# Optimization experiments

Hardware: AMD Instinct MI355X
Metric: run time of the kernel (lower is better)

The kernel has to match this reference:

```python
import jax, jax.numpy as jnp
import numpy as np

EPS = 1e-5

def layer_norm(x, alpha, beta):
    mean = jnp.mean(x, axis=-1, keepdims=True)
    var = jnp.mean(jnp.square(x - mean), axis=-1, keepdims=True)
    return alpha * ((x - mean) / jnp.sqrt(var + EPS)) + beta

def setup_inputs() -> dict:
    key = jax.random.key(0)
    B, S, D, H = 4, 2048, 1024, 16
    Dff = 4 * D
    ks = jax.random.split(key, 8)
    inp = {
        "x": jax.random.normal(ks[0], (B, S, D), jnp.float32),
        "attention_mask": jnp.ones((B, S), jnp.int32),
        "ln1_alpha": jnp.ones((D,), jnp.float32),
        "ln1_beta": jnp.zeros((D,), jnp.float32),
        "ln2_alpha": jnp.ones((D,), jnp.float32),
        "ln2_beta": jnp.zeros((D,), jnp.float32),
        "Wq": jax.random.normal(ks[1], (D, D), jnp.float32) * 0.05,
        "Wk": jax.random.normal(ks[2], (D, D), jnp.float32) * 0.05,
        "Wv": jax.random.normal(ks[3], (D, D), jnp.float32) * 0.05,
        "Wo": jax.random.normal(ks[4], (D, D), jnp.float32) * 0.05,
        "W1": jax.random.normal(ks[5], (D, Dff), jnp.float32) * 0.02,
        "b1": jnp.zeros((Dff,), jnp.float32),
        "W2": jax.random.normal(ks[6], (Dff, D), jnp.float32) * 0.02,
        "b2": jnp.zeros((D,), jnp.float32),
    }
    return inp

def reference(x, attention_mask, ln1_alpha, ln1_beta, ln2_alpha, ln2_beta,
              Wq, Wk, Wv, Wo, W1, b1, W2, b2):
    B, S, D = x.shape
    H = 16
    dh = D // H

    # LN1 + self-attention
    y = layer_norm(x, ln1_alpha, ln1_beta)
    Q = (y @ Wq).reshape(B, S, H, dh).transpose(0, 2, 1, 3)  # [B,H,S,dh]
    K = (y @ Wk).reshape(B, S, H, dh).transpose(0, 2, 1, 3)
    V = (y @ Wv).reshape(B, S, H, dh).transpose(0, 2, 1, 3)

    scores = jnp.einsum("bhqd,bhkd->bhqk", Q, K) / jnp.sqrt(jnp.float32(dh))
    causal = jnp.tril(jnp.ones((S, S), jnp.float32))  # [S,S]
    tmask = attention_mask.astype(jnp.float32)  # [B,S]
    amask = causal[None, None, :, :] * tmask[:, None, None, :] * tmask[:, None, :, None]
    scores = jnp.where(amask > 0, scores, jnp.float32(-1e30))
    attn = jax.nn.softmax(scores, axis=-1)
    # dropout omitted (deterministic inference)
    ctx = jnp.einsum("bhqk,bhkd->bhqd", attn, V)
    ctx = ctx.transpose(0, 2, 1, 3).reshape(B, S, D)
    x = x + ctx @ Wo

    # LN2 + GELU FFN
    y = layer_norm(x, ln2_alpha, ln2_beta)
    h = jax.nn.gelu(y @ W1 + b1, approximate=False)
    x = x + (h @ W2 + b2)
    return x
```

## Files before the change

kernel.cpp:

```cpp
#include <hip/hip_runtime.h>
#include <math.h>

typedef unsigned short u16;
typedef unsigned int u32;
typedef __attribute__((ext_vector_type(4))) unsigned short u16x4;
typedef __attribute__((ext_vector_type(8))) short bf16x8;
typedef __attribute__((ext_vector_type(4))) float f32x4;

#define B_ 4
#define S_ 2048
#define D_ 1024
#define H_ 16
#define NT (B_*S_)
#define DFF 4096

static __device__ __forceinline__ float bf2f(u16 u) {
    return __uint_as_float(((u32)u) << 16);
}
static __device__ __forceinline__ u16 f2bf(float f) {
    u32 u = __float_as_uint(f);
    u32 r = (u + 0x7fffu + ((u >> 16) & 1u)) >> 16;
    return (u16)r;
}
static __device__ __forceinline__ void gload_lds16(const void* g, void* l) {
    __builtin_amdgcn_global_load_lds(
        (const __attribute__((address_space(1))) void*)g,
        (__attribute__((address_space(3))) void*)l, 16, 0, 0);
}
static __device__ __forceinline__ float gelu_fast(float x) {
    float x2 = x * x;
    float u = x * fmaf(0.044715f, x2, 1.0f);
    float e = exp2f(2.3022079f * u);
    float r = __builtin_amdgcn_rcpf(e + 1.0f);
    return x - x * r;
}

#define MBAR() do { asm volatile("" ::: "memory"); \
                    __builtin_amdgcn_s_barrier(); \
                    asm volatile("" ::: "memory"); } while (0)

__global__ void transpose_f2b4(const float* __restrict__ s0, const float* __restrict__ s1,
                               const float* __restrict__ s2, const float* __restrict__ s3,
                               u16* __restrict__ d0, u16* __restrict__ d1,
                               u16* __restrict__ d2, u16* __restrict__ d3,
                               int R, int C) {
    const float* in = s0; u16* out = d0;
    if (blockIdx.z == 1) { in = s1; out = d1; }
    else if (blockIdx.z == 2) { in = s2; out = d2; }
    else if (blockIdx.z == 3) { in = s3; out = d3; }
    __shared__ float t[32][33];
    int c0 = blockIdx.x * 32, r0 = blockIdx.y * 32;
    int x = threadIdx.x, y = threadIdx.y;
    #pragma unroll
    for (int i = 0; i < 4; i++)
        t[y + i*8][x] = in[(long)(r0 + y + i*8) * C + c0 + x];
    __syncthreads();
    #pragma unroll
    for (int i = 0; i < 4; i++)
        out[(long)(c0 + y + i*8) * R + r0 + x] = f2bf(t[x][y + i*8]);
}

__global__ void transpose_f2b(const float* __restrict__ in, u16* __restrict__ out,
                              int R, int C) {
    __shared__ float t[32][33];
    int c0 = blockIdx.x * 32, r0 = blockIdx.y * 32;
    int x = threadIdx.x, y = threadIdx.y;
    #pragma unroll
    for (int i = 0; i < 4; i++)
        t[y + i*8][x] = in[(long)(r0 + y + i*8) * C + c0 + x];
    __syncthreads();
    #pragma unroll
    for (int i = 0; i < 4; i++)
        out[(long)(c0 + y + i*8) * R + r0 + x] = f2bf(t[x][y + i*8]);
}

__global__ void transpose_v(const u16* __restrict__ V, u16* __restrict__ Vt) {
    __shared__ u16 t[32][33];
    int z = blockIdx.z; int b = z >> 4, h = z & 15;
    int s0 = blockIdx.x * 32, d0 = blockIdx.y * 32;
    int x = threadIdx.x, y = threadIdx.y;
    const u16* in = V + ((long)b * S_ + s0) * D_ + h * 64 + d0;
    #pragma unroll
    for (int i = 0; i < 4; i++)
        t[y + i*8][x] = in[(long)(y + i*8) * D_ + x];
    __syncthreads();
    u16* out = Vt + ((long)z * 64 + d0) * S_ + s0;
    #pragma unroll
    for (int i = 0; i < 4; i++)
        out[(long)(y + i*8) * S_ + x] = t[x][y + i*8];
}

__global__ __launch_bounds__(256) void ln_kernel(
    const float* __restrict__ X, const float* __restrict__ alpha,
    const float* __restrict__ beta, u16* __restrict__ Y) {
    int row = blockIdx.x, tid = threadIdx.x;
    float4 xv = ((const float4*)(X + (long)row * D_))[tid];
    float v[4] = {xv.x, xv.y, xv.z, xv.w};
    float s = 0.f, ss = 0.f;
    #pragma unroll
    for (int i = 0; i < 4; i++) { s += v[i]; ss += v[i]*v[i]; }
    #pragma unroll
    for (int off = 32; off >= 1; off >>= 1) {
        s += __shfl_xor(s, off);
        ss += __shfl_xor(ss, off);
    }
    __shared__ float red[8];
    __shared__ float stats[2];
    int w = tid >> 6;
    if ((tid & 63) == 0) { red[w] = s; red[4 + w] = ss; }
    __syncthreads();
    if (tid == 0) {
        float S = red[0] + red[1] + red[2] + red[3];
        float SS = red[4] + red[5] + red[6] + red[7];
        float mean = S * (1.f / D_);
        float var = SS * (1.f / D_) - mean * mean;
        stats[0] = mean; stats[1] = rsqrtf(var + 1e-5f);
    }
    __syncthreads();
    float mean = stats[0], rstd = stats[1];
    float4 av = ((const float4*)alpha)[tid];
    float4 bv = ((const float4*)beta)[tid];
    u16x4 o;
    o[0] = f2bf((v[0] - mean) * rstd * av.x + bv.x);
    o[1] = f2bf((v[1] - mean) * rstd * av.y + bv.y);
    o[2] = f2bf((v[2] - mean) * rstd * av.z + bv.z);
    o[3] = f2bf((v[3] - mean) * rstd * av.w + bv.w);
    *(u16x4*)(Y + (long)row * D_ + tid * 4) = o;
}

#define BM 128
#define BN 128
#define BK 64

__global__ __launch_bounds__(256, 3) void gemm_bt(
    const u16* __restrict__ A,
    const u16* __restrict__ Bt0, const u16* __restrict__ Bt1, const u16* __restrict__ Bt2,
    void* __restrict__ C0, void* __restrict__ C1, void* __restrict__ C2,
    int M, int N, int K, int mode,
    const float* __restrict__ bias, const float* __restrict__ resid) {
    const u16* Bt = Bt0; void* C = C0;
    if (blockIdx.z == 1) { Bt = Bt1; C = C1; }
    else if (blockIdx.z == 2) { Bt = Bt2; C = C2; }

    __shared__ __align__(16) u16 Asm[BM * BK];
    __shared__ __align__(16) u16 Bsm[BN * BK];

    int tid = threadIdx.x;
    int lane = tid & 63, wave = tid >> 6;
    int l15 = lane & 15, quad = lane >> 4;
    int wm = wave & 1, wn = wave >> 1;
    long tm0 = (long)blockIdx.y * BM, tn0 = (long)blockIdx.x * BN;

    int srow = lane >> 3;
    int scol = (lane & 7) * 8;

    f32x4 acc[4][4] = {};

    for (int k0 = 0; k0 < K; k0 += BK) {
        __syncthreads();
        #pragma unroll
        for (int c = 0; c < 4; c++) {
            int chunk = wave * 4 + c;
            int row = chunk * 8 + srow;
            gload_lds16(&A[(tm0 + row) * (long)K + k0 + scol], &Asm[chunk * 512]);
            gload_lds16(&Bt[(tn0 + row) * (long)K + k0 + scol], &Bsm[chunk * 512]);
        }
        __syncthreads();
        #pragma unroll
        for (int ks = 0; ks < 2; ks++) {
            bf16x8 af[4], bfm[4];
            #pragma unroll
            for (int mt = 0; mt < 4; mt++)
                af[mt] = *(const bf16x8*)&Asm[(wm*64 + mt*16 + l15) * BK + ks*32 + quad*8];
            #pragma unroll
            for (int nt = 0; nt < 4; nt++)
                bfm[nt] = *(const bf16x8*)&Bsm[(wn*64 + nt*16 + l15) * BK + ks*32 + quad*8];
            #pragma unroll
            for (int mt = 0; mt < 4; mt++)
                #pragma unroll
                for (int nt = 0; nt < 4; nt++)
                    acc[mt][nt] = __builtin_amdgcn_mfma_f32_16x16x32_bf16(
                        af[mt], bfm[nt], acc[mt][nt], 0, 0, 0);
        }
    }

    #pragma unroll
    for (int mt = 0; mt < 4; mt++) {
        #pragma unroll
        for (int nt = 0; nt < 4; nt++) {
            #pragma unroll
            for (int i = 0; i < 4; i++) {
                long r = tm0 + wm*64 + mt*16 + quad*4 + i;
                long cn = tn0 + wn*64 + nt*16 + l15;
                long idx = r * N + cn;
                float val = acc[mt][nt][i];
                if (mode == 0) {
                    ((u16*)C)[idx] = f2bf(val);
                } else if (mode == 1) {
                    ((float*)C)[idx] = val + resid[idx];
                } else if (mode == 2) {
                    val += bias[cn];
                    ((u16*)C)[idx] = f2bf(gelu_fast(val));
                } else {
                    ((float*)C)[idx] = val + bias[cn] + resid[idx];
                }
            }
        }
    }
}

#define BM2 256
#define BN2 256
#define BK2 64

__global__ __launch_bounds__(512, 2) void gemm8p(
    const u16* __restrict__ A, const u16* __restrict__ Bt,
    u16* __restrict__ C0, u16* __restrict__ C1, u16* __restrict__ C2,
    int N, int K, int mode, const float* __restrict__ bias) {
    __shared__ __align__(16) u16 lds[2 * 32768];

    int tid = threadIdx.x;
    int lane = tid & 63, wave = tid >> 6;
    int l15 = lane & 15, quad = lane >> 4;
    int wm = wave & 1, wn = wave >> 1;
    long tm0 = (long)blockIdx.y * BM2, tn0 = (long)blockIdx.x * BN2;
    int srow = lane >> 3;
    int scolw = ((lane & 7) ^ srow) * 8;
    int sk = l15 & 7;
    int ca0 = ((quad) ^ sk) * 8;
    int ca1 = ((4 + quad) ^ sk) * 8;
    int steps = K >> 6;

    auto STAGE = [&](int kt, int half, int buf) {
        long kk = (long)kt * BK2;
        #pragma unroll
        for (int c = 0; c < 2; c++) {
            int chunk = wave * 2 + c;
            int rloc = (half & 1) * 128 + chunk * 8 + srow;
            const u16* g = (half < 2)
                ? &A [(tm0 + rloc) * (long)K + kk + scolw]
                : &Bt[(tn0 + rloc) * (long)K + kk + scolw];
            u16* l = &lds[buf * 32768 + (half >= 2 ? 16384 : 0)
                          + (half & 1) * 8192 + chunk * 512];
            gload_lds16(g, l);
        }
    };

    f32x4 acc[8][4] = {};
    bf16x8 af[4][2], bl[2][2], bh[2][2];

    STAGE(0, 0, 0); STAGE(0, 1, 0); STAGE(0, 2, 0); STAGE(0, 3, 0);
    if (steps > 1) { STAGE(1, 2, 1); STAGE(1, 3, 1); }
    if (steps > 1) asm volatile("s_waitcnt vmcnt(4)" ::: "memory");
    else           asm volatile("s_waitcnt vmcnt(0)" ::: "memory");
    MBAR();

    for (int t = 0; t < steps; ++t) {
        int cur = t & 1;
        const u16* Ab = &lds[cur * 32768];
        const u16* Bb = &lds[cur * 32768 + 16384];
        bool pf1 = (t + 1 < steps), pf2 = (t + 2 < steps);

        #pragma unroll
        for (int mt = 0; mt < 4; mt++) {
            int row = wm*128 + mt*16 + l15;
            af[mt][0] = *(const bf16x8*)&Ab[row * BK2 + ca0];
            af[mt][1] = *(const bf16x8*)&Ab[row * BK2 + ca1];
        }
        #pragma unroll
        for (int nt = 0; nt < 2; nt++) {
            int row = wn*64 + nt*16 + l15;
            bl[nt][0] = *(const bf16x8*)&Bb[row * BK2 + ca0];
            bl[nt][1] = *(const bf16x8*)&Bb[row * BK2 + ca1];
        }
        if (pf1) STAGE(t + 1, 0, cur ^ 1);
        MBAR();
        __builtin_amdgcn_s_setprio(1);
        #pragma unroll
        for (int mt = 0; mt < 4; mt++)
            #pragma unroll
            for (int nt = 0; nt < 2; nt++) {
                acc[mt][nt] = __builtin_amdgcn_mfma_f32_16x16x32_bf16(af[mt][0], bl[nt][0], acc[mt][nt], 0,0,0);
                acc[mt][nt] = __builtin_amdgcn_mfma_f32_16x16x32_bf16(af[mt][1], bl[nt][1], acc[mt][nt], 0,0,0);
            }
        __builtin_amdgcn_s_setprio(0);
        MBAR();

        #pragma unroll
        for (int nt = 0; nt < 2; nt++) {
            int row = wn*64 + (2+nt)*16 + l15;
            bh[nt][0] = *(const bf16x8*)&Bb[row * BK2 + ca0];
            bh[nt][1] = *(const bf16x8*)&Bb[row * BK2 + ca1];
        }
        if (pf1) STAGE(t + 1, 1, cur ^ 1);
        MBAR();
        __builtin_amdgcn_s_setprio(1);
        #pragma unroll
        for (int mt = 0; mt < 4; mt++)
            #pragma unroll
            for (int nt = 0; nt < 2; nt++) {
                acc[mt][2+nt] = __builtin_amdgcn_mfma_f32_16x16x32_bf16(af[mt][0], bh[nt][0], acc[mt][2+nt], 0,0,0);
                acc[mt][2+nt] = __builtin_amdgcn_mfma_f32_16x16x32_bf16(af[mt][1], bh[nt][1], acc[mt][2+nt], 0,0,0);
            }
        __builtin_amdgcn_s_setprio(0);
        MBAR();

        #pragma unroll
        for (int mt = 0; mt < 4; mt++) {
            int row = wm*128 + 64 + mt*16 + l15;
            af[mt][0] = *(const bf16x8*)&Ab[row * BK2 + ca0];
            af[mt][1] = *(const bf16x8*)&Ab[row * BK2 + ca1];
        }
        if (pf2) STAGE(t + 2, 2, cur);
        MBAR();
        __builtin_amdgcn_s_setprio(1);
        #pragma unroll
        for (int mt = 0; mt < 4; mt++)
            #pragma unroll
            for (int nt = 0; nt < 2; nt++) {
                acc[4+mt][2+nt] = __builtin_amdgcn_mfma_f32_16x16x32_bf16(af[mt][0], bh[nt][0], acc[4+mt][2+nt], 0,0,0);
                acc[4+mt][2+nt] = __builtin_amdgcn_mfma_f32_16x16x32_bf16(af[mt][1], bh[nt][1], acc[4+mt][2+nt], 0,0,0);
            }
        __builtin_amdgcn_s_setprio(0);
        MBAR();

        if (pf2) STAGE(t + 2, 3, cur);
        MBAR();
        __builtin_amdgcn_s_setprio(1);
        #pragma unroll
        for (int mt = 0; mt < 4; mt++)
            #pragma unroll
            for (int nt = 0; nt < 2; nt++) {
                acc[4+mt][nt] = __builtin_amdgcn_mfma_f32_16x16x32_bf16(af[mt][0], bl[nt][0], acc[4+mt][nt], 0,0,0);
                acc[4+mt][nt] = __builtin_amdgcn_mfma_f32_16x16x32_bf16(af[mt][1], bl[nt][1], acc[4+mt][nt], 0,0,0);
            }
        __builtin_amdgcn_s_setprio(0);
        if (pf2) asm volatile("s_waitcnt vmcnt(4)" ::: "memory");
        else     asm volatile("s_waitcnt vmcnt(0)" ::: "memory");
        MBAR();
    }

    #pragma unroll
    for (int mt = 0; mt < 8; mt++) {
        #pragma unroll
        for (int nt = 0; nt < 4; nt++) {
            #pragma unroll
            for (int i = 0; i < 4; i++) {
                long r = tm0 + wm*128 + mt*16 + quad*4 + i;
                int cn = (int)tn0 + wn*64 + nt*16 + l15;
                float val = acc[mt][nt][i];
                if (mode == 0) {
                    int mi = cn >> 10;
                    int col = cn & 1023;
                    u16* base = (mi == 0) ? C0 : (mi == 1 ? C1 : C2);
                    base[r * 1024 + col] = f2bf(val);
                } else {
                    val += bias[cn];
                    C0[r * (long)N + cn] = f2bf(gelu_fast(val));
                }
            }
        }
    }
}

#define LDP 72

__global__ __launch_bounds__(128, 2) void attn_kernel(
    const u16* __restrict__ Q, const u16* __restrict__ Kg, const u16* __restrict__ Vt,
    const int* __restrict__ mask, u16* __restrict__ O) {
    __shared__ __align__(16) u16 Psm[2][32 * LDP];
    int tid = threadIdx.x;
    int lane = tid & 63, wave = tid >> 6;
    int l15 = lane & 15, quad = lane >> 4;
    int bh = blockIdx.x; int b = bh >> 4, h = bh & 15;
    int j = blockIdx.y * 2 + wave;
    long tokBase = (long)b * S_;
    const float SCL = 0.125f * 1.4426950408889634f;
    const float MMAX = 20.0f;

    const bf16x8 ones = {16256,16256,16256,16256,16256,16256,16256,16256};
    u16* Pw = Psm[wave];
    const int* mb = mask + b * S_;

    #pragma unroll
    for (int half = 0; half < 2; half++) {
        int t = half ? (63 - j) : j;
        int q0 = t * 32;

        bf16x8 aq[2][2];
        #pragma unroll
        for (int mt = 0; mt < 2; mt++) {
            const u16* qptr = Q + (tokBase + q0 + mt*16 + l15) * D_ + h * 64;
            aq[mt][0] = *(const bf16x8*)(qptr + quad * 8);
            aq[mt][1] = *(const bf16x8*)(qptr + 32 + quad * 8);
        }

        f32x4 o[2][4] = {};
        f32x4 lacc[2] = {};
        int ktiles = t / 2 + 1;

        bf16x8 kb[4][2];
        #pragma unroll
        for (int nt = 0; nt < 4; nt++) {
            const u16* kp = Kg + (tokBase + nt*16 + l15) * D_ + h * 64;
            kb[nt][0] = *(const bf16x8*)(kp + quad * 8);
            kb[nt][1] = *(const bf16x8*)(kp + 32 + quad * 8);
        }

        for (int kt = 0; kt < ktiles; kt++) {
            int k0 = kt * 64;
            bf16x8 vb[4][2];
            #pragma unroll
            for (int d = 0; d < 4; d++) {
                const u16* vp = Vt + ((long)bh * 64 + d*16 + l15) * S_ + k0;
                vb[d][0] = *(const bf16x8*)(vp + quad * 8);
                vb[d][1] = *(const bf16x8*)(vp + 32 + quad * 8);
            }

            f32x4 s[2][4] = {};
            #pragma unroll
            for (int nt = 0; nt < 4; nt++) {
                s[0][nt] = __builtin_amdgcn_mfma_f32_16x16x32_bf16(aq[0][0], kb[nt][0], s[0][nt], 0,0,0);
                s[0][nt] = __builtin_amdgcn_mfma_f32_16x16x32_bf16(aq[0][1], kb[nt][1], s[0][nt], 0,0,0);
                s[1][nt] = __builtin_amdgcn_mfma_f32_16x16x32_bf16(aq[1][0], kb[nt][0], s[1][nt], 0,0,0);
                s[1][nt] = __builtin_amdgcn_mfma_f32_16x16x32_bf16(aq[1][1], kb[nt][1], s[1][nt], 0,0,0);
            }

            int k1 = (kt + 1 < ktiles) ? k0 + 64 : k0;
            bf16x8 kbn[4][2];
            #pragma unroll
            for (int nt = 0; nt < 4; nt++) {
                const u16* kp = Kg + (tokBase + k1 + nt*16 + l15) * D_ + h * 64;
                kbn[nt][0] = *(const bf16x8*)(kp + quad * 8);
                kbn[nt][1] = *(const bf16x8*)(kp + 32 + quad * 8);
            }

            int mk = 0;
            #pragma unroll
            for (int nt = 0; nt < 4; nt++)
                if (mb[k0 + nt*16 + l15] != 0) mk |= (1 << nt);

            #pragma unroll
            for (int mt = 0; mt < 2; mt++) {
                #pragma unroll
                for (int i = 0; i < 4; i++) {
                    int qq = q0 + mt*16 + quad*4 + i;
                    #pragma unroll
                    for (int nt = 0; nt < 4; nt++) {
                        int kc = k0 + nt*16 + l15;
                        float p = exp2f(fmaf(s[mt][nt][i], SCL, -MMAX));
                        p = (kc <= qq && ((mk >> nt) & 1)) ? p : 0.f;
                        Pw[(mt*16 + quad*4 + i) * LDP + nt*16 + l15] = f2bf(p);
                    }
                }
            }
            asm volatile("s_waitcnt lgkmcnt(0)" ::: "memory");

            #pragma unroll
            for (int hv = 0; hv < 2; hv++) {
                bf16x8 ap0 = *(const bf16x8*)&Pw[l15 * LDP + hv*32 + quad*8];
                bf16x8 ap1 = *(const bf16x8*)&Pw[(16 + l15) * LDP + hv*32 + quad*8];
                #pragma unroll
                for (int d = 0; d < 4; d++) {
                    o[0][d] = __builtin_amdgcn_mfma_f32_16x16x32_bf16(ap0, vb[d][hv], o[0][d], 0,0,0);
                    o[1][d] = __builtin_amdgcn_mfma_f32_16x16x32_bf16(ap1, vb[d][hv], o[1][d], 0,0,0);
                }
                lacc[0] = __builtin_amdgcn_mfma_f32_16x16x32_bf16(ap0, ones, lacc[0], 0,0,0);
                lacc[1] = __builtin_amdgcn_mfma_f32_16x16x32_bf16(ap1, ones, lacc[1], 0,0,0);
            }

            #pragma unroll
            for (int nt = 0; nt < 4; nt++) {
                kb[nt][0] = kbn[nt][0];
                kb[nt][1] = kbn[nt][1];
            }
        }

        #pragma unroll
        for (int mt = 0; mt < 2; mt++) {
            #pragma unroll
            for (int i = 0; i < 4; i++) {
                float inv = 1.f / lacc[mt][i];
                long r = tokBase + q0 + mt*16 + quad*4 + i;
                #pragma unroll
                for (int d = 0; d < 4; d++)
                    O[r * D_ + h*64 + d*16 + l15] = f2bf(o[mt][d][i] * inv);
            }
        }
    }
}

extern "C" void kernel_launch(void* const* d_in, const int* in_sizes, int n_in,
                              void* d_out, int out_size, void* d_ws, size_t ws_size,
                              hipStream_t stream) {
    const float* x    = (const float*)d_in[0];
    const int*   am   = (const int*)d_in[1];
    const float* ln1a = (const float*)d_in[2];
    const float* ln1b = (const float*)d_in[3];
    const float* ln2a = (const float*)d_in[4];
    const float* ln2b = (const float*)d_in[5];
    const float* wq   = (const float*)d_in[6];
    const float* wk   = (const float*)d_in[7];
    const float* wv   = (const float*)d_in[8];
    const float* wo   = (const float*)d_in[9];
    const float* w1   = (const float*)d_in[10];
    const float* b1   = (const float*)d_in[11];
    const float* w2   = (const float*)d_in[12];
    const float* b2   = (const float*)d_in[13];
    float* out = (float*)d_out;

    char* ws = (char*)d_ws;
    const size_t MB16 = (size_t)16 * 1024 * 1024;
    u16* y1      = (u16*)(ws + 0 * MB16);
    u16* q       = (u16*)(ws + 1 * MB16);
    u16* k       = (u16*)(ws + 2 * MB16);
    u16* v       = (u16*)(ws + 3 * MB16);
    u16* wqt     = (u16*)(ws + 4 * MB16 + 0 * (size_t)D_ * D_ * 2);
    u16* wkt     = (u16*)(ws + 4 * MB16 + 1 * (size_t)D_ * D_ * 2);
    u16* wvt     = (u16*)(ws + 4 * MB16 + 2 * (size_t)D_ * D_ * 2);
    u16* wot     = (u16*)(ws + 4 * MB16 + 3 * (size_t)D_ * D_ * 2);
    u16* y2      = y1;
    u16* w1t     = q;
    u16* w2t     = q + (size_t)D_ * DFF;
    u16* h_full  = k;
    u16* ctx     = v;
    u16*   vt  = (u16*)d_out;
    float* x1f = out;

    dim3 tb(32, 8);
    transpose_f2b4<<<dim3(D_/32, D_/32, 4), tb, 0, stream>>>(
        wq, wk, wv, wo, wqt, wkt, wvt, wot, D_, D_);

    ln_kernel<<<NT, 256, 0, stream>>>(x, ln1a, ln1b, y1);

    gemm8p<<<dim3(3*D_/BN2, NT/BM2), 512, 0, stream>>>(
        y1, wqt, q, k, v, 3*D_, D_, 0, nullptr);

    transpose_v<<<dim3(S_/32, 2, B_*H_), tb, 0, stream>>>(v, vt);

    attn_kernel<<<dim3(B_*H_, 16), 128, 0, stream>>>(q, k, vt, am, ctx);

    gemm_bt<<<dim3(D_/BN, NT/BM, 1), 256, 0, stream>>>(
        ctx, wot, wot, wot, x1f, x1f, x1f, NT, D_, D_, 1, nullptr, x);

    transpose_f2b<<<dim3(DFF/32, D_/32), tb, 0, stream>>>(w1, w1t, D_, DFF);
    transpose_f2b<<<dim3(D_/32, DFF/32), tb, 0, stream>>>(w2, w2t, DFF, D_);

    ln_kernel<<<NT, 256, 0, stream>>>(x1f, ln2a, ln2b, y2);

    gemm8p<<<dim3(DFF/BN2, NT/BM2), 512, 0, stream>>>(
        y2, w1t, h_full, h_full, h_full, DFF, D_, 2, b1);
    gemm_bt<<<dim3(D_/BN, NT/BM, 1), 256, 0, stream>>>(
        h_full, w2t, w2t, w2t, out, out, out, NT, D_, DFF, 3, b2, x1f);
}
```

Before: 630.1 us.

## Use pipelined 256x128 GEMM for W2 projection and software-pipeline attention QK

Adds a new 512-thread, double-buffered 256x128-tile GEMM kernel with bias and residual epilogue and uses it for the final FFN down-projection in place of the generic gemm_bt. It also restructures the attention inner loop so the QK^T MFMAs for the next key tile are issued before the current tile's PV MFMAs, overlapping score computation with the softmax/LDS work. The aim is better MFMA utilisation and latency hiding. The cost is higher register pressure from the extra score accumulators, which could hurt occupancy.

Measured after the change: 622.2 us. About the same (-1.3%).

```diff
diff --git a/kernel.cpp b/kernel.cpp
--- a/kernel.cpp
+++ b/kernel.cpp
@@ -363,6 +363,140 @@
     }
 }
 
+__global__ __launch_bounds__(512, 2) void gemm8p_n128(
+    const u16* __restrict__ A, const u16* __restrict__ Bt,
+    float* __restrict__ C, int N, int K,
+    const float* __restrict__ bias, const float* __restrict__ resid) {
+    __shared__ __align__(16) u16 lds[2 * 24576];
+
+    int tid = threadIdx.x;
+    int lane = tid & 63, wave = tid >> 6;
+    int l15 = lane & 15, quad = lane >> 4;
+    int wm = wave & 1, wn = wave >> 1;
+    long tm0 = (long)blockIdx.y * 256, tn0 = (long)blockIdx.x * 128;
+    int srow = lane >> 3;
+    int scolw = ((lane & 7) ^ srow) * 8;
+    int sk = l15 & 7;
+    int ca0 = ((quad) ^ sk) * 8;
+    int ca1 = ((4 + quad) ^ sk) * 8;
+    int steps = K >> 6;
+
+    auto STAGE = [&](int kt, int half, int buf) {
+        long kk = (long)kt * 64;
+        if (half < 2) {
+            #pragma unroll
+            for (int c = 0; c < 2; c++) {
+                int chunk = wave * 2 + c;
+                int rloc = half * 128 + chunk * 8 + srow;
+                gload_lds16(&A[(tm0 + rloc) * (long)K + kk + scolw],
+                            &lds[buf * 24576 + half * 8192 + chunk * 512]);
+            }
+        } else {
+            int rloc = (half - 2) * 64 + wave * 8 + srow;
+            gload_lds16(&Bt[(tn0 + rloc) * (long)K + kk + scolw],
+                        &lds[buf * 24576 + 16384 + (half - 2) * 4096 + wave * 512]);
+        }
+    };
+
+    f32x4 acc[8][2] = {};
+    bf16x8 af[4][2], bl[2], bh[2];
+
+    STAGE(0, 0, 0); STAGE(0, 1, 0); STAGE(0, 2, 0); STAGE(0, 3, 0);
+    if (steps > 1) { STAGE(1, 2, 1); STAGE(1, 3, 1); }
+    if (steps > 1) asm volatile("s_waitcnt vmcnt(2)" ::: "memory");
+    else           asm volatile("s_waitcnt vmcnt(0)" ::: "memory");
+    MBAR();
+
+    for (int t = 0; t < steps; ++t) {
+        int cur = t & 1;
+        const u16* Ab = &lds[cur * 24576];
+        const u16* Bb = &lds[cur * 24576 + 16384];
+        bool pf1 = (t + 1 < steps), pf2 = (t + 2 < steps);
+
+        #pragma unroll
+        for (int mt = 0; mt < 4; mt++) {
+            int row = wm*128 + mt*16 + l15;
+            af[mt][0] = *(const bf16x8*)&Ab[row * 64 + ca0];
+            af[mt][1] = *(const bf16x8*)&Ab[row * 64 + ca1];
+        }
+        {
+            int row = wn*32 + l15;
+            bl[0] = *(const bf16x8*)&Bb[row * 64 + ca0];
+            bl[1] = *(const bf16x8*)&Bb[row * 64 + ca1];
+        }
+        if (pf1) STAGE(t + 1, 0, cur ^ 1);
+        MBAR();
+        __builtin_amdgcn_s_setprio(1);
+        #pragma unroll
+        for (int mt = 0; mt < 4; mt++) {
+            acc[mt][0] = __builtin_amdgcn_mfma_f32_16x16x32_bf16(af[mt][0], bl[0], acc[mt][0], 0,0,0);
+            acc[mt][0] = __builtin_amdgcn_mfma_f32_16x16x32_bf16(af[mt][1], bl[1], acc[mt][0], 0,0,0);
+        }
+        __builtin_amdgcn_s_setprio(0);
+        MBAR();
+
+        {
+            int row = wn*32 + 16 + l15;
+            bh[0] = *(const bf16x8*)&Bb[row * 64 + ca0];
+            bh[1] = *(const bf16x8*)&Bb[row * 64 + ca1];
+        }
+        if (pf1) STAGE(t + 1, 1, cur ^ 1);
+        MBAR();
+        __builtin_amdgcn_s_setprio(1);
+        #pragma unroll
+        for (int mt = 0; mt < 4; mt++) {
+            acc[mt][1] = __builtin_amdgcn_mfma_f32_16x16x32_bf16(af[mt][0], bh[0], acc[mt][1], 0,0,0);
+            acc[mt][1] = __builtin_amdgcn_mfma_f32_16x16x32_bf16(af[mt][1], bh[1], acc[mt][1], 0,0,0);
+        }
+        __builtin_amdgcn_s_setprio(0);
+        MBAR();
+
+        #pragma unroll
+        for (int mt = 0; mt < 4; mt++) {
+            int row = wm*128 + 64 + mt*16 + l15;
+            af[mt][0] = *(const bf16x8*)&Ab[row * 64 + ca0];
+            af[mt][1] = *(const bf16x8*)&Ab[row * 64 + ca1];
+        }
+        if (pf2) STAGE(t + 2, 2, cur);
+        MBAR();
+        __builtin_amdgcn_s_setprio(1);
+        #pragma unroll
+        for (int mt = 0; mt < 4; mt++) {
+            acc[4+mt][1] = __builtin_amdgcn_mfma_f32_16x16x32_bf16(af[mt][0], bh[0], acc[4+mt][1], 0,0,0);
+            acc[4+mt][1] = __builtin_amdgcn_mfma_f32_16x16x32_bf16(af[mt][1], bh[1], acc[4+mt][1], 0,0,0);
+        }
+        __builtin_amdgcn_s_setprio(0);
+        MBAR();
+
+        if (pf2) STAGE(t + 2, 3, cur);
+        MBAR();
+        __builtin_amdgcn_s_setprio(1);
+        #pragma unroll
+        for (int mt = 0; mt < 4; mt++) {
+            acc[4+mt][0] = __builtin_amdgcn_mfma_f32_16x16x32_bf16(af[mt][0], bl[0], acc[4+mt][0], 0,0,0);
+            acc[4+mt][0] = __builtin_amdgcn_mfma_f32_16x16x32_bf16(af[mt][1], bl[1], acc[4+mt][0], 0,0,0);
+        }
+        __builtin_amdgcn_s_setprio(0);
+        if (pf2) asm volatile("s_waitcnt vmcnt(2)" ::: "memory");
+        else     asm volatile("s_waitcnt vmcnt(0)" ::: "memory");
+        MBAR();
+    }
+
+    #pragma unroll
+    for (int mt = 0; mt < 8; mt++) {
+        #pragma unroll
+        for (int nt = 0; nt < 2; nt++) {
+            #pragma unroll
+            for (int i = 0; i < 4; i++) {
+                long r = tm0 + wm*128 + mt*16 + quad*4 + i;
+                int cn = (int)tn0 + wn*32 + nt*16 + l15;
+                long idx = r * (long)N + cn;
+                C[idx] = acc[mt][nt][i] + bias[cn] + resid[idx];
+            }
+        }
+    }
+}
+
 #define LDP 72
 
 __global__ __launch_bounds__(128, 2) void attn_kernel(
@@ -406,6 +540,14 @@
             kb[nt][0] = *(const bf16x8*)(kp + quad * 8);
             kb[nt][1] = *(const bf16x8*)(kp + 32 + quad * 8);
         }
+        f32x4 s[2][4] = {};
+        #pragma unroll
+        for (int nt = 0; nt < 4; nt++) {
+            s[0][nt] = __builtin_amdgcn_mfma_f32_16x16x32_bf16(aq[0][0], kb[nt][0], s[0][nt], 0,0,0);
+            s[0][nt] = __builtin_amdgcn_mfma_f32_16x16x32_bf16(aq[0][1], kb[nt][1], s[0][nt], 0,0,0);
+            s[1][nt] = __builtin_amdgcn_mfma_f32_16x16x32_bf16(aq[1][0], kb[nt][0], s[1][nt], 0,0,0);
+            s[1][nt] = __builtin_amdgcn_mfma_f32_16x16x32_bf16(aq[1][1], kb[nt][1], s[1][nt], 0,0,0);
+        }
 
         for (int kt = 0; kt < ktiles; kt++) {
             int k0 = kt * 64;
@@ -416,23 +558,12 @@
                 vb[d][0] = *(const bf16x8*)(vp + quad * 8);
                 vb[d][1] = *(const bf16x8*)(vp + 32 + quad * 8);
             }
-
-            f32x4 s[2][4] = {};
-            #pragma unroll
-            for (int nt = 0; nt < 4; nt++) {
-                s[0][nt] = __builtin_amdgcn_mfma_f32_16x16x32_bf16(aq[0][0], kb[nt][0], s[0][nt], 0,0,0);
-                s[0][nt] = __builtin_amdgcn_mfma_f32_16x16x32_bf16(aq[0][1], kb[nt][1], s[0][nt], 0,0,0);
-                s[1][nt] = __builtin_amdgcn_mfma_f32_16x16x32_bf16(aq[1][0], kb[nt][0], s[1][nt], 0,0,0);
-                s[1][nt] = __builtin_amdgcn_mfma_f32_16x16x32_bf16(aq[1][1], kb[nt][1], s[1][nt], 0,0,0);
-            }
-
             int k1 = (kt + 1 < ktiles) ? k0 + 64 : k0;
-            bf16x8 kbn[4][2];
             #pragma unroll
             for (int nt = 0; nt < 4; nt++) {
                 const u16* kp = Kg + (tokBase + k1 + nt*16 + l15) * D_ + h * 64;
-                kbn[nt][0] = *(const bf16x8*)(kp + quad * 8);
-                kbn[nt][1] = *(const bf16x8*)(kp + 32 + quad * 8);
+                kb[nt][0] = *(const bf16x8*)(kp + quad * 8);
+                kb[nt][1] = *(const bf16x8*)(kp + 32 + quad * 8);
             }
 
             int mk = 0;
@@ -454,6 +585,18 @@
                     }
                 }
             }
+
+            f32x4 sn[2][4] = {};
+            if (kt + 1 < ktiles) {
+                #pragma unroll
+                for (int nt = 0; nt < 4; nt++) {
+                    sn[0][nt] = __builtin_amdgcn_mfma_f32_16x16x32_bf16(aq[0][0], kb[nt][0], sn[0][nt], 0,0,0);
+                    sn[0][nt] = __builtin_amdgcn_mfma_f32_16x16x32_bf16(aq[0][1], kb[nt][1], sn[0][nt], 0,0,0);
+                    sn[1][nt] = __builtin_amdgcn_mfma_f32_16x16x32_bf16(aq[1][0], kb[nt][0], sn[1][nt], 0,0,0);
+                    sn[1][nt] = __builtin_amdgcn_mfma_f32_16x16x32_bf16(aq[1][1], kb[nt][1], sn[1][nt], 0,0,0);
+                }
+            }
+
             asm volatile("s_waitcnt lgkmcnt(0)" ::: "memory");
 
             #pragma unroll
@@ -470,10 +613,10 @@
             }
 
             #pragma unroll
-            for (int nt = 0; nt < 4; nt++) {
-                kb[nt][0] = kbn[nt][0];
-                kb[nt][1] = kbn[nt][1];
-            }
+            for (int mt = 0; mt < 2; mt++)
+                #pragma unroll
+                for (int nt = 0; nt < 4; nt++)
+                    s[mt][nt] = sn[mt][nt];
         }
 
         #pragma unroll
@@ -550,6 +693,7 @@
 
     gemm8p<<<dim3(DFF/BN2, NT/BM2), 512, 0, stream>>>(
         y2, w1t, h_full, h_full, h_full, DFF, D_, 2, b1);
-    gemm_bt<<<dim3(D_/BN, NT/BM, 1), 256, 0, stream>>>(
-        h_full, w2t, w2t, w2t, out, out, out, NT, D_, DFF, 3, b2, x1f);
-}
+
+    gemm8p_n128<<<dim3(D_/128, NT/256), 512, 0, stream>>>(
+        h_full, w2t, out, D_, DFF, b2, x1f);
+}
```
